# Performance work log

Hardware: AMD Instinct MI355X
Metric: run time of the kernel (lower is better)

The kernel has to match this reference:

```python
import jax, jax.numpy as jnp
from jax import lax
import numpy as np

NPOINT, RADIUS, NSAMPLE = 512, 0.2, 32
BN_EPS = 1e-5


def _index_points(points, idx):
    # points: [B, N, C]; idx: [B, ...] int -> [B, ..., C]
    return jax.vmap(lambda p, i: p[i])(points, idx)


def _farthest_point_sample(xyz, npoint):
    # xyz: [B, N, 3] -> [B, npoint] int32 (deterministic start at index 0)
    B, N, _ = xyz.shape
    def step(carry, _):
        distance, farthest = carry  # [B,N], [B]
        centroid = xyz[jnp.arange(B), farthest]            # [B,3]
        d = jnp.sum((xyz - centroid[:, None, :]) ** 2, -1)  # [B,N]
        distance = jnp.minimum(distance, d)
        nxt = jnp.argmax(distance, axis=-1).astype(jnp.int32)
        return (distance, nxt), farthest
    init = (jnp.full((B, N), 1e10, xyz.dtype), jnp.zeros((B,), jnp.int32))
    _, idxs = lax.scan(step, init, None, length=npoint)
    return idxs.T  # [B, npoint]


def _query_ball_point(radius, nsample, xyz, new_xyz):
    # xyz: [B,N,3], new_xyz: [B,S,3] -> [B,S,nsample] int32
    B, N, _ = xyz.shape
    S = new_xyz.shape[1]
    # squared distances [B,S,N]
    sqrdists = (jnp.sum(new_xyz ** 2, -1)[:, :, None]
                + jnp.sum(xyz ** 2, -1)[:, None, :]
                - 2.0 * jnp.einsum('bsc,bnc->bsn', new_xyz, xyz))
    group_idx = jnp.broadcast_to(jnp.arange(N, dtype=jnp.int32), (B, S, N))
    group_idx = jnp.where(sqrdists > radius * radius, N, group_idx)
    group_idx = jnp.sort(group_idx, axis=-1)[:, :, :nsample]
    first = group_idx[:, :, :1]
    return jnp.where(group_idx == N, first, group_idx)


def _mlp_layer(x, w, b, g, be):
    # x: [B, Cin, K, S]; 1x1 conv + BatchNorm2d (training stats) + relu
    y = jnp.einsum('bcks,oc->boks', x, w) + b[None, :, None, None]
    mean = jnp.mean(y, axis=(0, 2, 3), keepdims=True)
    var = jnp.mean((y - mean) ** 2, axis=(0, 2, 3), keepdims=True)
    y = (y - mean) * lax.rsqrt(var + BN_EPS)
    y = y * g[None, :, None, None] + be[None, :, None, None]
    return jax.nn.relu(y)


def setup_inputs() -> dict:
    key = jax.random.key(0)
    ks = jax.random.split(key, 16)
    inp = {
        'xyz': jax.random.uniform(ks[0], (8, 3, 16384), jnp.float32),
        'points': jax.random.normal(ks[1], (8, 3, 16384), jnp.float32),
    }
    chans = [6, 64, 64, 128]
    for i in range(3):
        cin, cout = chans[i], chans[i + 1]
        inp[f'w{i}'] = jax.random.normal(ks[2 + 4 * i], (cout, cin), jnp.float32) / np.float32(np.sqrt(cin))
        inp[f'b{i}'] = jax.random.normal(ks[3 + 4 * i], (cout,), jnp.float32) * 0.01
        inp[f'g{i}'] = jnp.ones((cout,), jnp.float32)
        inp[f'be{i}'] = jnp.zeros((cout,), jnp.float32)
    return inp


def reference(xyz, points, w0, b0, g0, be0, w1, b1, g1, be1, w2, b2, g2, be2):
    xyz_t = jnp.transpose(xyz, (0, 2, 1))      # [B,N,3]
    pts_t = jnp.transpose(points, (0, 2, 1))   # [B,N,D]
    B, N, C = xyz_t.shape

    fps_idx = _farthest_point_sample(xyz_t, NPOINT)        # [B,S]
    new_xyz = _index_points(xyz_t, fps_idx)                # [B,S,3]
    group_idx = _query_ball_point(RADIUS, NSAMPLE, xyz_t, new_xyz)  # [B,S,K]
    grouped_xyz = _index_points(xyz_t, group_idx) - new_xyz[:, :, None, :]  # [B,S,K,3]
    grouped_pts = _index_points(pts_t, group_idx)          # [B,S,K,D]
    new_points = jnp.concatenate([grouped_pts, grouped_xyz], axis=-1)  # [B,S,K,D+3]

    x = jnp.transpose(new_points, (0, 3, 2, 1))  # [B, C, K, S]
    for (w, b, g, be) in ((w0, b0, g0, be0), (w1, b1, g1, be1), (w2, b2, g2, be2)):
        x = _mlp_layer(x, w, b, g, be)
    new_feat = jnp.max(x, axis=2)                # [B, 128, S]
    new_xyz_out = jnp.transpose(new_xyz, (0, 2, 1))  # [B, 3, S]
    return (new_xyz_out, new_feat)
```

## Files before the change

kernel.cpp:

```cpp
#include <hip/hip_runtime.h>
#include <cstdint>
#include <cstddef>

#define BB 8
#define NN 16384
#define SS 512
#define KK 32

__device__ __forceinline__ float fm(float a, float b){ return __fmul_rn(a,b); }
__device__ __forceinline__ float fa(float a, float b){ return __fadd_rn(a,b); }
__device__ __forceinline__ float fsb(float a, float b){ return __fsub_rn(a,b); }

__global__ void sqnorm_kernel(const float* __restrict__ xyz, float* __restrict__ sqn){
  int gid = blockIdx.x*blockDim.x + threadIdx.x;
  int b = gid >> 14; int n = gid & (NN-1);
  const float* xb = xyz + (size_t)b*3*NN;
  float x = xb[n], y = xb[NN+n], z = xb[2*NN+n];
  sqn[gid] = fa(fa(fm(x,x),fm(y,y)),fm(z,z));
}

__global__ __launch_bounds__(1024, 4) void fps_kernel(const float* __restrict__ xyz,
                                                      float* __restrict__ nxyz,
                                                      float* __restrict__ out)
{
  int b = blockIdx.x;
  int t = threadIdx.x;
  const float* xb = xyz + (size_t)b*3*NN;
  float px[16], py[16], pz[16], dist[16];
#pragma unroll
  for (int k=0;k<16;k++){
    int n = k*1024 + t;
    px[k]=xb[n]; py[k]=xb[NN+n]; pz[k]=xb[2*NN+n];
    dist[k]=1e10f;
  }
  __shared__ unsigned long long redk[2][16];
  int wid = t >> 6, lane = t & 63;
  float cx = xb[0], cy = xb[NN], cz = xb[2*NN];
  for (int step=0; step<SS; ++step){
    if (t==0){
      float* nx = nxyz + ((size_t)b*SS + step)*3;
      nx[0]=cx; nx[1]=cy; nx[2]=cz;
      float* ox = out + (size_t)b*3*SS;
      ox[step]=cx; ox[SS+step]=cy; ox[2*SS+step]=cz;
    }
    float bv = -1.0f; int bk = 0;
#pragma unroll
    for (int k=0;k<16;k++){
      float dx=fsb(px[k],cx), dy=fsb(py[k],cy), dz=fsb(pz[k],cz);
      float d = fa(fa(fm(dx,dx),fm(dy,dy)),fm(dz,dz));
      float dk = fminf(dist[k], d);
      dist[k]=dk;
      if (dk > bv){ bv=dk; bk=k; }
    }
    int bi = (bk<<10) | t;
    unsigned long long key = ((unsigned long long)__float_as_uint(bv) << 32)
                           | (unsigned)(16384 - bi);
#pragma unroll
    for (int off=1; off<64; off<<=1){
      unsigned long long ok = __shfl_xor(key, off);
      if (ok > key) key = ok;
    }
    int par = step & 1;
    if (lane==0) redk[par][wid] = key;
    __syncthreads();
    unsigned long long k2 = redk[par][lane & 15];
#pragma unroll
    for (int off=1; off<16; off<<=1){
      unsigned long long ok = __shfl_xor(k2, off);
      if (ok > k2) k2 = ok;
    }
    int i = 16384 - (int)(unsigned)(k2 & 0xFFFFFFFFull);
    cx = xb[i]; cy = xb[NN+i]; cz = xb[2*NN+i];
  }
}

__global__ void ballq_kernel(const float* __restrict__ xyz,
                             const float* __restrict__ sqn,
                             const float* __restrict__ nxyz,
                             int* __restrict__ gidx)
{
  int wv = (blockIdx.x * (blockDim.x>>6)) + (threadIdx.x>>6);
  int lane = threadIdx.x & 63;
  int b = wv >> 9; int s = wv & (SS-1);
  const float* nx3 = nxyz + ((size_t)b*SS + s)*3;
  float nx=nx3[0], ny=nx3[1], nz=nx3[2];
  float cn = fa(fa(fm(nx,nx),fm(ny,ny)),fm(nz,nz));
  const float* xb = xyz + (size_t)b*3*NN;
  const float* sb = sqn + (size_t)b*NN;
  const float R2 = (float)(0.2*0.2);
  int* g = gidx + ((size_t)b*SS + s)*KK;
  int cnt = 0; int first_idx = 0;
  for (int base=0; base<NN; base+=64){
    int n = base + lane;
    float x=xb[n], y=xb[NN+n], z=xb[2*NN+n];
    float dot = fa(fa(fm(nx,x),fm(ny,y)),fm(nz,z));
    float sqd = fsb(fa(cn, sb[n]), fm(2.0f, dot));
    bool inb = !(sqd > R2);
    unsigned long long m = __ballot(inb);
    if (m){
      if (cnt==0) first_idx = base + __builtin_ctzll(m);
      int pre = __popcll(m & ((1ull<<lane)-1ull));
      int slot = cnt + pre;
      if (inb && slot < KK) g[slot] = n;
      cnt += __popcll(m);
      if (cnt >= KK) break;
    }
  }
  if (cnt < KK && lane >= cnt && lane < KK) g[lane] = first_idx;
}

__global__ __launch_bounds__(256) void mlp0_kernel(const float* __restrict__ xyz,
                            const float* __restrict__ pts,
                            const float* __restrict__ nxyz,
                            const int* __restrict__ gidx,
                            const float* __restrict__ w,
                            const float* __restrict__ bias,
                            float* __restrict__ y0)
{
  int gid = blockIdx.x*blockDim.x + threadIdx.x;
  int b = gid / (KK*SS);
  int r = gid % (KK*SS);
  int k = r / SS; int s = r % SS;
  int idx = gidx[((size_t)b*SS + s)*KK + k];
  const float* pb = pts + (size_t)b*3*NN;
  const float* xb = xyz + (size_t)b*3*NN;
  const float* nx3 = nxyz + ((size_t)b*SS + s)*3;
  float in[6];
  in[0]=pb[idx]; in[1]=pb[NN+idx]; in[2]=pb[2*NN+idx];
  in[3]=xb[idx]-nx3[0]; in[4]=xb[NN+idx]-nx3[1]; in[5]=xb[2*NN+idx]-nx3[2];
  float* po = y0 + (size_t)b*64*KK*SS + r;
  for (int o=0;o<64;o++){
    float acc = bias[o];
#pragma unroll
    for (int c=0;c<6;c++) acc += in[c]*w[o*6+c];
    po[(size_t)o*KK*SS] = acc;
  }
}

__global__ __launch_bounds__(256) void stats_part_kernel(const float* __restrict__ y, int C,
                                                         double* __restrict__ psum)
{
  int o = blockIdx.x >> 3; int b = blockIdx.x & 7;
  int t = threadIdx.x;
  const float4* p = (const float4*)(y + ((size_t)b*C + o)*KK*SS);
  double s1=0.0, s2=0.0;
#pragma unroll
  for (int i=0;i<16;i++){
    float4 v = p[t + i*256];
    double x0=v.x, x1=v.y, x2=v.z, x3=v.w;
    s1 += x0+x1; s1 += x2+x3;
    s2 += x0*x0 + x1*x1;
    s2 += x2*x2 + x3*x3;
  }
#pragma unroll
  for (int off=32; off>=1; off>>=1){
    s1 += __shfl_down(s1, off);
    s2 += __shfl_down(s2, off);
  }
  __shared__ double l1[4], l2[4];
  int wid = t>>6;
  if ((t&63)==0){ l1[wid]=s1; l2[wid]=s2; }
  __syncthreads();
  if (t==0){
    double t1=l1[0]+l1[1]+l1[2]+l1[3];
    double t2=l2[0]+l2[1]+l2[2]+l2[3];
    psum[(o*8+b)*2+0]=t1;
    psum[(o*8+b)*2+1]=t2;
  }
}

__global__ void stats_fin_kernel(const double* __restrict__ psum, int C,
                                 const float* __restrict__ gamma,
                                 const float* __restrict__ beta,
                                 float* __restrict__ a, float* __restrict__ c)
{
  int o = threadIdx.x;
  if (o >= C) return;
  double t1=0.0, t2=0.0;
#pragma unroll
  for (int b=0;b<8;b++){ t1 += psum[(o*8+b)*2+0]; t2 += psum[(o*8+b)*2+1]; }
  double n = (double)BB*KK*SS;
  double m = t1/n;
  double var = t2/n - m*m;
  double inv = 1.0/sqrt(var + 1e-5);
  float sc = (float)((double)gamma[o]*inv);
  a[o]=sc; c[o]=(float)((double)beta[o] - m*(double)sc);
}

template<int CIN, int COUT>
__global__ __launch_bounds__(256) void mlp_kernel(const float* __restrict__ yin,
                            const float* __restrict__ w,
                            const float* __restrict__ bias,
                            const float* __restrict__ a,
                            const float* __restrict__ cc,
                            float* __restrict__ yout)
{
  int gid = blockIdx.x*blockDim.x + threadIdx.x;
  int b = gid / (KK*SS);
  int r = gid % (KK*SS);
  const float* pin = yin + (size_t)b*CIN*KK*SS + r;
  float x[CIN];
#pragma unroll
  for (int ci=0;ci<CIN;ci++) x[ci] = fmaxf(fmaf(pin[(size_t)ci*KK*SS], a[ci], cc[ci]), 0.0f);
  float* po = yout + (size_t)b*COUT*KK*SS + r;
  for (int o=0;o<COUT;o++){
    float acc = bias[o];
#pragma unroll
    for (int ci=0;ci<CIN;ci++) acc += x[ci]*w[o*CIN+ci];
    po[(size_t)o*KK*SS] = acc;
  }
}

__global__ __launch_bounds__(256) void final_kernel(const float* __restrict__ y2,
                             const float* __restrict__ a,
                             const float* __restrict__ cc,
                             float* __restrict__ out)
{
  int gid = blockIdx.x*blockDim.x + threadIdx.x;
  int b = gid / (128*128);
  int r = gid % (128*128);
  int o = r >> 7; int s4 = (r & 127);
  const float4* p = (const float4*)(y2 + ((size_t)b*128 + o)*KK*SS) + s4;
  float sc=a[o], sh=cc[o];
  float m0=0.f,m1=0.f,m2=0.f,m3=0.f;
#pragma unroll
  for (int k=0;k<KK;k++){
    float4 v = p[k*(SS/4)];
    m0 = fmaxf(m0, fmaxf(fmaf(v.x, sc, sh), 0.0f));
    m1 = fmaxf(m1, fmaxf(fmaf(v.y, sc, sh), 0.0f));
    m2 = fmaxf(m2, fmaxf(fmaf(v.z, sc, sh), 0.0f));
    m3 = fmaxf(m3, fmaxf(fmaf(v.w, sc, sh), 0.0f));
  }
  float4* po = (float4*)(out + ((size_t)b*128 + o)*SS) + s4;
  *po = make_float4(m0,m1,m2,m3);
}

extern "C" void kernel_launch(void* const* d_in, const int* in_sizes, int n_in,
                              void* d_out, int out_size, void* d_ws, size_t ws_size,
                              hipStream_t stream)
{
  const float* xyz = (const float*)d_in[0];
  const float* pts = (const float*)d_in[1];
  const float* w0  = (const float*)d_in[2];
  const float* b0  = (const float*)d_in[3];
  const float* g0  = (const float*)d_in[4];
  const float* be0 = (const float*)d_in[5];
  const float* w1  = (const float*)d_in[6];
  const float* b1  = (const float*)d_in[7];
  const float* g1  = (const float*)d_in[8];
  const float* be1 = (const float*)d_in[9];
  const float* w2  = (const float*)d_in[10];
  const float* b2  = (const float*)d_in[11];
  const float* g2  = (const float*)d_in[12];
  const float* be2 = (const float*)d_in[13];
  float* out = (float*)d_out;

  char* ws = (char*)d_ws;
  float*  sqn  = (float*) (ws + 0);
  float*  nxyz = (float*) (ws + 524288);
  int*    gidx = (int*)   (ws + 573440);
  float*  st   = (float*) (ws + 1097728);
  double* ps0  = (double*)(ws + 1099776);
  double* ps1  = (double*)(ws + 1107968);
  double* ps2  = (double*)(ws + 1116160);
  float* a0=st,     *c0=st+64;
  float* a1=st+128, *c1=st+192;
  float* a2=st+256, *c2=st+384;
  float* y1 = (float*)(ws + 4194304);
  float* y2 = (float*)(ws + 41943040);
  float* y0 = (float*)(ws + 79691776);
  (void)ws_size; (void)in_sizes; (void)n_in; (void)out_size;

  sqnorm_kernel<<<dim3(512), dim3(256), 0, stream>>>(xyz, sqn);
  fps_kernel<<<dim3(BB), dim3(1024), 0, stream>>>(xyz, nxyz, out);
  ballq_kernel<<<dim3(1024), dim3(256), 0, stream>>>(xyz, sqn, nxyz, gidx);
  mlp0_kernel<<<dim3(512), dim3(256), 0, stream>>>(xyz, pts, nxyz, gidx, w0, b0, y0);
  stats_part_kernel<<<dim3(64*8), dim3(256), 0, stream>>>(y0, 64, ps0);
  stats_fin_kernel<<<dim3(1), dim3(64), 0, stream>>>(ps0, 64, g0, be0, a0, c0);
  mlp_kernel<64,64><<<dim3(512), dim3(256), 0, stream>>>(y0, w1, b1, a0, c0, y1);
  stats_part_kernel<<<dim3(64*8), dim3(256), 0, stream>>>(y1, 64, ps1);
  stats_fin_kernel<<<dim3(1), dim3(64), 0, stream>>>(ps1, 64, g1, be1, a1, c1);
  mlp_kernel<64,128><<<dim3(512), dim3(256), 0, stream>>>(y1, w2, b2, a1, c1, y2);
  stats_part_kernel<<<dim3(128*8), dim3(256), 0, stream>>>(y2, 128, ps2);
  stats_fin_kernel<<<dim3(1), dim3(128), 0, stream>>>(ps2, 128, g2, be2, a2, c2);
  final_kernel<<<dim3(512), dim3(256), 0, stream>>>(y2, a2, c2, out + BB*3*SS);
}
```

Measured before the change: 1.306 ms.

## Split farthest point sampling across four blocks per batch with global-memory handshake

Result: slower. 1.618 ms (+24.0%).

```diff
diff --git a/kernel.cpp b/kernel.cpp
--- a/kernel.cpp
+++ b/kernel.cpp
@@ -7,12 +7,17 @@
 #define SS 512
 #define KK 32
 
+#define FPB 4
+#define PPT 4
+
 __device__ __forceinline__ float fm(float a, float b){ return __fmul_rn(a,b); }
 __device__ __forceinline__ float fa(float a, float b){ return __fadd_rn(a,b); }
 __device__ __forceinline__ float fsb(float a, float b){ return __fsub_rn(a,b); }
 
-__global__ void sqnorm_kernel(const float* __restrict__ xyz, float* __restrict__ sqn){
+__global__ void sqnorm_kernel(const float* __restrict__ xyz, float* __restrict__ sqn,
+                              unsigned long long* __restrict__ comm){
   int gid = blockIdx.x*blockDim.x + threadIdx.x;
+  if (blockIdx.x==0 && threadIdx.x < 128) comm[threadIdx.x] = 0ull;
   int b = gid >> 14; int n = gid & (NN-1);
   const float* xb = xyz + (size_t)b*3*NN;
   float x = xb[n], y = xb[NN+n], z = xb[2*NN+n];
@@ -21,15 +26,19 @@
 
 __global__ __launch_bounds__(1024, 4) void fps_kernel(const float* __restrict__ xyz,
                                                       float* __restrict__ nxyz,
-                                                      float* __restrict__ out)
-{
-  int b = blockIdx.x;
+                                                      float* __restrict__ out,
+                                                      unsigned long long* __restrict__ comm)
+{
+  int blk = blockIdx.x;
+  int b = blk & 7;
+  int j = blk >> 3;
   int t = threadIdx.x;
   const float* xb = xyz + (size_t)b*3*NN;
-  float px[16], py[16], pz[16], dist[16];
-#pragma unroll
-  for (int k=0;k<16;k++){
-    int n = k*1024 + t;
+  const int base = j*(NN/FPB);
+  float px[PPT], py[PPT], pz[PPT], dist[PPT];
+#pragma unroll
+  for (int k=0;k<PPT;k++){
+    int n = base + k*1024 + t;
     px[k]=xb[n]; py[k]=xb[NN+n]; pz[k]=xb[2*NN+n];
     dist[k]=1e10f;
   }
@@ -37,7 +46,7 @@
   int wid = t >> 6, lane = t & 63;
   float cx = xb[0], cy = xb[NN], cz = xb[2*NN];
   for (int step=0; step<SS; ++step){
-    if (t==0){
+    if (j==0 && t==0){
       float* nx = nxyz + ((size_t)b*SS + step)*3;
       nx[0]=cx; nx[1]=cy; nx[2]=cz;
       float* ox = out + (size_t)b*3*SS;
@@ -45,16 +54,16 @@
     }
     float bv = -1.0f; int bk = 0;
 #pragma unroll
-    for (int k=0;k<16;k++){
+    for (int k=0;k<PPT;k++){
       float dx=fsb(px[k],cx), dy=fsb(py[k],cy), dz=fsb(pz[k],cz);
       float d = fa(fa(fm(dx,dx),fm(dy,dy)),fm(dz,dz));
       float dk = fminf(dist[k], d);
       dist[k]=dk;
       if (dk > bv){ bv=dk; bk=k; }
     }
-    int bi = (bk<<10) | t;
+    int n_mine = base + (bk<<10) + t;
     unsigned long long key = ((unsigned long long)__float_as_uint(bv) << 32)
-                           | (unsigned)(16384 - bi);
+                           | (unsigned)(16384 - n_mine);
 #pragma unroll
     for (int off=1; off<64; off<<=1){
       unsigned long long ok = __shfl_xor(key, off);
@@ -63,13 +72,41 @@
     int par = step & 1;
     if (lane==0) redk[par][wid] = key;
     __syncthreads();
-    unsigned long long k2 = redk[par][lane & 15];
-#pragma unroll
-    for (int off=1; off<16; off<<=1){
-      unsigned long long ok = __shfl_xor(k2, off);
-      if (ok > k2) k2 = ok;
-    }
-    int i = 16384 - (int)(unsigned)(k2 & 0xFFFFFFFFull);
+    if (wid==0){
+      unsigned long long k2 = redk[par][lane & 15];
+#pragma unroll
+      for (int off=1; off<16; off<<=1){
+        unsigned long long ok = __shfl_xor(k2, off);
+        if (ok > k2) k2 = ok;
+      }
+      if (lane==0){
+        unsigned long long d32 = k2 >> 32;
+        unsigned idx = 16384u - (unsigned)(k2 & 0xFFFFFFFFull);
+        unsigned long long w = (d32<<32)
+                             | ((unsigned long long)(16383u - idx) << 18)
+                             | (unsigned)(step+1);
+        __hip_atomic_store(&comm[(size_t)(par*8 + b)*8 + j], w,
+                           __ATOMIC_RELAXED, __HIP_MEMORY_SCOPE_AGENT);
+      }
+    }
+    const unsigned tag = (unsigned)(step+1);
+    const unsigned long long* cm = comm + (size_t)(par*8 + b)*8;
+    unsigned long long w0,w1,w2,w3;
+    for(;;){
+      w0 = __hip_atomic_load(cm+0, __ATOMIC_RELAXED, __HIP_MEMORY_SCOPE_AGENT);
+      w1 = __hip_atomic_load(cm+1, __ATOMIC_RELAXED, __HIP_MEMORY_SCOPE_AGENT);
+      w2 = __hip_atomic_load(cm+2, __ATOMIC_RELAXED, __HIP_MEMORY_SCOPE_AGENT);
+      w3 = __hip_atomic_load(cm+3, __ATOMIC_RELAXED, __HIP_MEMORY_SCOPE_AGENT);
+      if ( ((unsigned)(w0 & 0x3FFFFull) == tag) &&
+           ((unsigned)(w1 & 0x3FFFFull) == tag) &&
+           ((unsigned)(w2 & 0x3FFFFull) == tag) &&
+           ((unsigned)(w3 & 0x3FFFFull) == tag) ) break;
+      __builtin_amdgcn_s_sleep(1);
+    }
+    unsigned long long g0 = w0 > w1 ? w0 : w1;
+    unsigned long long g1 = w2 > w3 ? w2 : w3;
+    unsigned long long g  = g0 > g1 ? g0 : g1;
+    int i = 16383 - (int)((g >> 18) & 0x3FFFull);
     cx = xb[i]; cy = xb[NN+i]; cz = xb[2*NN+i];
   }
 }
@@ -263,6 +300,7 @@
   double* ps0  = (double*)(ws + 1099776);
   double* ps1  = (double*)(ws + 1107968);
   double* ps2  = (double*)(ws + 1116160);
+  unsigned long long* comm = (unsigned long long*)(ws + 1132544);
   float* a0=st,     *c0=st+64;
   float* a1=st+128, *c1=st+192;
   float* a2=st+256, *c2=st+384;
@@ -271,8 +309,8 @@
   float* y0 = (float*)(ws + 79691776);
   (void)ws_size; (void)in_sizes; (void)n_in; (void)out_size;
 
-  sqnorm_kernel<<<dim3(512), dim3(256), 0, stream>>>(xyz, sqn);
-  fps_kernel<<<dim3(BB), dim3(1024), 0, stream>>>(xyz, nxyz, out);
+  sqnorm_kernel<<<dim3(512), dim3(256), 0, stream>>>(xyz, sqn, comm);
+  fps_kernel<<<dim3(BB*FPB), dim3(1024), 0, stream>>>(xyz, nxyz, out, comm);
   ballq_kernel<<<dim3(1024), dim3(256), 0, stream>>>(xyz, sqn, nxyz, gidx);
   mlp0_kernel<<<dim3(512), dim3(256), 0, stream>>>(xyz, pts, nxyz, gidx, w0, b0, y0);
   stats_part_kernel<<<dim3(64*8), dim3(256), 0, stream>>>(y0, 64, ps0);
```
